# Performance work log

Hardware: AMD Instinct MI355X
Metric: run time of the kernel (lower is better)

Reference implementation:

```python
import jax, jax.numpy as jnp
import numpy as np

N_NODES = 100000
EPS = 1e-12  # F.normalize eps


def mean_aggregate(x, src, dst):
    # gather source features along edges, segment-mean into destinations
    msg = x[src]                                              # [E, D]
    summed = jax.ops.segment_sum(msg, dst, num_segments=N_NODES)  # [N, D]
    cnt = jax.ops.segment_sum(jnp.ones_like(dst, dtype=x.dtype), dst,
                              num_segments=N_NODES)           # [N]
    return summed / jnp.maximum(cnt, 1.0)[:, None]


def sage_conv(x, src, dst, W_l, b_l, W_r, normalize):
    agg = mean_aggregate(x, src, dst)
    out = agg @ W_l.T + b_l + x @ W_r.T  # lin_l(mean neigh) + lin_r(root)
    if normalize:
        norm = jnp.sqrt(jnp.sum(out * out, axis=-1, keepdims=True))
        out = out / jnp.maximum(norm, EPS)
    return out


def setup_inputs() -> dict:
    key = jax.random.key(0)
    ks = jax.random.split(key, 8)
    H, O = 128, 128
    s = 1.0 / np.sqrt(H)
    x = jax.random.normal(ks[0], (N_NODES, H), dtype=jnp.float32)
    edge_index = jax.random.randint(ks[1], (2, 1600000), 0, N_NODES, dtype=jnp.int64)
    return {
        "x": x,
        "edge_index": edge_index,
        "W1l": jax.random.uniform(ks[2], (H, H), jnp.float32, -s, s),
        "b1": jax.random.uniform(ks[3], (H,), jnp.float32, -s, s),
        "W1r": jax.random.uniform(ks[4], (H, H), jnp.float32, -s, s),
        "W2l": jax.random.uniform(ks[5], (O, H), jnp.float32, -s, s),
        "b2": jax.random.uniform(ks[6], (O,), jnp.float32, -s, s),
        "W2r": jax.random.uniform(ks[7], (O, H), jnp.float32, -s, s),
    }


def reference(x, edge_index, W1l, b1, W1r, W2l, b2, W2r):
    src, dst = edge_index[0], edge_index[1]
    h = sage_conv(x, src, dst, W1l, b1, W1r, normalize=True)
    h = jax.nn.relu(h)
    out = sage_conv(h, src, dst, W2l, b2, W2r, normalize=False)
    return out
```

## Files before the change

kernel.cpp:

```cpp
#include <hip/hip_runtime.h>
#include <hip/hip_bf16.h>
#include <hip/hip_fp16.h>

#define N_NODES 100000
#define DFEAT 128
#define SLAB 4096
#define BSHIFT 9
#define NBUCK 196

#define WS_CNT      0
#define WS_W16      100000
#define WS_BCNT     180000
#define WS_BBASE    180200
#define WS_BCUR     180400
#define WS_OFFS     200000
#define WS_ESRC     300608
#define WS_AGGH     1900608
#define WS_CASTH    8300608

typedef _Float16 half8 __attribute__((ext_vector_type(8)));
typedef _Float16 half2v __attribute__((ext_vector_type(2)));
typedef float floatx4 __attribute__((ext_vector_type(4)));

__global__ __launch_bounds__(256) void prep_kernel(const float* __restrict__ x,
                                                   __half* __restrict__ xh, int total4,
                                                   const int* __restrict__ dst,
                                                   int* __restrict__ bcnt,
                                                   const float* __restrict__ W1l,
                                                   const float* __restrict__ W1r,
                                                   const float* __restrict__ W2l,
                                                   const float* __restrict__ W2r,
                                                   __half* __restrict__ w16,
                                                   int E, int bpart, int castblocks) {
    __shared__ int lh[NBUCK];
    int b = blockIdx.x;
    if (b < castblocks) {
        int i = b * 256 + threadIdx.x;
        if (i < total4) {
            float4 v = ((const float4*)x)[i];
            __half2 h01 = __floats2half2_rn(v.x, v.y);
            __half2 h23 = __floats2half2_rn(v.z, v.w);
            uint2 o;
            o.x = *(unsigned int*)&h01;
            o.y = *(unsigned int*)&h23;
            ((uint2*)xh)[i] = o;
        }
        return;
    }
    if (b < castblocks + 64) {
        int i = (b - castblocks) * 256 + threadIdx.x;
        int m = i >> 12;
        int off = i & 4095;
        const float* Wp = (m == 0) ? W1l : (m == 1) ? W1r : (m == 2) ? W2l : W2r;
        float4 v = ((const float4*)Wp)[off];
        __half2 h01 = __floats2half2_rn(v.x, v.y);
        __half2 h23 = __floats2half2_rn(v.z, v.w);
        uint2 o;
        o.x = *(unsigned int*)&h01;
        o.y = *(unsigned int*)&h23;
        ((uint2*)w16)[i] = o;
        return;
    }
    int bb = b - castblocks - 64;
    for (int i = threadIdx.x; i < NBUCK; i += 256) lh[i] = 0;
    __syncthreads();
    int s0 = bb * SLAB, s1 = min(E, s0 + SLAB);
    for (int i = s0 + threadIdx.x; i < s1; i += 256)
        atomicAdd(&lh[dst[i] >> BSHIFT], 1);
    __syncthreads();
    for (int i = threadIdx.x; i < NBUCK; i += 256)
        if (lh[i] > 0) atomicAdd(&bcnt[i], lh[i]);
}

__global__ void bscan_kernel(const int* __restrict__ bcnt, int* __restrict__ bbase,
                             int* __restrict__ bcur, int E) {
    __shared__ int s[256];
    int t = threadIdx.x;
    int v = (t < NBUCK) ? bcnt[t] : 0;
    s[t] = v;
    __syncthreads();
    for (int d = 1; d < 256; d <<= 1) {
        int u = (t >= d) ? s[t - d] : 0;
        __syncthreads();
        s[t] += u;
        __syncthreads();
    }
    if (t < NBUCK) {
        int excl = s[t] - v;
        bbase[t] = excl;
        bcur[t] = excl;
    }
    if (t == 0) bbase[NBUCK] = E;
}

__global__ __launch_bounds__(256) void phase2_kernel(const int* __restrict__ src,
                                                     const int* __restrict__ dst,
                                                     int* __restrict__ bcur,
                                                     int2* __restrict__ pairs,
                                                     int E) {
    __shared__ int lbase[NBUCK];
    __shared__ int lcur[NBUCK];
    __shared__ int lgb[NBUCK];
    __shared__ int sc[256];
    __shared__ int2 lp[SLAB];
    int b = blockIdx.x;
    int t = threadIdx.x;
    for (int i = t; i < NBUCK; i += 256) lbase[i] = 0;
    __syncthreads();
    int s0 = b * SLAB, s1 = min(E, s0 + SLAB);
    for (int i = s0 + t; i < s1; i += 256)
        atomicAdd(&lbase[dst[i] >> BSHIFT], 1);
    __syncthreads();
    int v = (t < NBUCK) ? lbase[t] : 0;
    sc[t] = v;
    __syncthreads();
    for (int d = 1; d < 256; d <<= 1) {
        int u = (t >= d) ? sc[t - d] : 0;
        __syncthreads();
        sc[t] += u;
        __syncthreads();
    }
    if (t < NBUCK) {
        int excl = sc[t] - v;
        lbase[t] = excl;
        lcur[t] = excl;
        lgb[t] = (v > 0) ? atomicAdd(&bcur[t], v) : 0;
    }
    __syncthreads();
    for (int i = s0 + t; i < s1; i += 256) {
        int d = dst[i];
        int s = src[i];
        int bk = d >> BSHIFT;
        int pos = atomicAdd(&lcur[bk], 1);
        lp[pos] = make_int2(s, d);
    }
    __syncthreads();
    int m = s1 - s0;
    for (int i = t; i < m; i += 256) {
        int2 p = lp[i];
        int bk = p.y >> BSHIFT;
        pairs[lgb[bk] + (i - lbase[bk])] = p;
    }
}

__global__ __launch_bounds__(512) void phase3_kernel(const int2* __restrict__ pairs,
                                                     const int* __restrict__ bbase,
                                                     int* __restrict__ cnt,
                                                     int* __restrict__ offs,
                                                     int* __restrict__ esrc,
                                                     int n) {
    __shared__ int lcnt[512];
    __shared__ int sc[512];
    __shared__ int lexcl[512];
    int g = blockIdx.x;
    int node0 = g << BSHIFT;
    int t = threadIdx.x;
    lcnt[t] = 0;
    __syncthreads();
    int S = bbase[g];
    int Eg = bbase[g + 1];
    for (int i = S + t; i < Eg; i += 512)
        atomicAdd(&lcnt[pairs[i].y - node0], 1);
    __syncthreads();
    int v = lcnt[t];
    sc[t] = v;
    __syncthreads();
    for (int d = 1; d < 512; d <<= 1) {
        int u = (t >= d) ? sc[t - d] : 0;
        __syncthreads();
        sc[t] += u;
        __syncthreads();
    }
    int excl = sc[t] - v;
    lexcl[t] = excl;
    int nd = node0 + t;
    if (nd < n) {
        cnt[nd] = v;
        offs[nd] = S + excl;
    }
    __syncthreads();
    for (int i = S + t; i < Eg; i += 512) {
        int2 p = pairs[i];
        int pos = atomicAdd(&lexcl[p.y - node0], 1);
        esrc[S + pos] = p.x;
    }
}

#define ACC(c, r)                        \
    s[c][0] += *(half2v*)&(r).x;         \
    s[c][1] += *(half2v*)&(r).y;         \
    s[c][2] += *(half2v*)&(r).z;         \
    s[c][3] += *(half2v*)&(r).w;

__global__ void aggregate_kernel(const __half* __restrict__ feat, const int* __restrict__ esrc,
                                 const int* __restrict__ offs, const int* __restrict__ cnt,
                                 __half* __restrict__ agg, int n) {
    int wid = (blockIdx.x * blockDim.x + threadIdx.x) >> 6;
    int lane = threadIdx.x & 63;
    int grp = lane >> 4;
    int l15 = lane & 15;
    int node = wid * 4 + grp;
    if (node >= n) return;
    int beg = offs[node];
    int deg = cnt[node];
    const _Float16* fbase = (const _Float16*)feat + l15 * 8;
    const int* ep = esrc + beg;

    half2v s[4][4];
#pragma unroll
    for (int c = 0; c < 4; c++)
#pragma unroll
        for (int k = 0; k < 4; k++) s[c][k] = (half2v)(_Float16)0;

    int j = 0;
    for (; j + 8 <= deg; j += 8) {
        int i0 = ep[j + 0], i1 = ep[j + 1], i2 = ep[j + 2], i3 = ep[j + 3];
        int i4 = ep[j + 4], i5 = ep[j + 5], i6 = ep[j + 6], i7 = ep[j + 7];
        uint4 r0 = *(const uint4*)(fbase + (size_t)i0 * DFEAT);
        uint4 r1 = *(const uint4*)(fbase + (size_t)i1 * DFEAT);
        uint4 r2 = *(const uint4*)(fbase + (size_t)i2 * DFEAT);
        uint4 r3 = *(const uint4*)(fbase + (size_t)i3 * DFEAT);
        uint4 r4 = *(const uint4*)(fbase + (size_t)i4 * DFEAT);
        uint4 r5 = *(const uint4*)(fbase + (size_t)i5 * DFEAT);
        uint4 r6 = *(const uint4*)(fbase + (size_t)i6 * DFEAT);
        uint4 r7 = *(const uint4*)(fbase + (size_t)i7 * DFEAT);
        ACC(0, r0) ACC(1, r1) ACC(2, r2) ACC(3, r3)
        ACC(0, r4) ACC(1, r5) ACC(2, r6) ACC(3, r7)
    }
    for (; j + 4 <= deg; j += 4) {
        int i0 = ep[j + 0], i1 = ep[j + 1], i2 = ep[j + 2], i3 = ep[j + 3];
        uint4 r0 = *(const uint4*)(fbase + (size_t)i0 * DFEAT);
        uint4 r1 = *(const uint4*)(fbase + (size_t)i1 * DFEAT);
        uint4 r2 = *(const uint4*)(fbase + (size_t)i2 * DFEAT);
        uint4 r3 = *(const uint4*)(fbase + (size_t)i3 * DFEAT);
        ACC(0, r0) ACC(1, r1) ACC(2, r2) ACC(3, r3)
    }
    if (j < deg) {
        int rem = deg - j;
        int i0 = ep[j];
        int i1 = ep[j + (rem > 1 ? 1 : 0)];
        int i2 = ep[j + (rem > 2 ? 2 : 0)];
        uint4 r0 = *(const uint4*)(fbase + (size_t)i0 * DFEAT);
        uint4 r1 = *(const uint4*)(fbase + (size_t)i1 * DFEAT);
        uint4 r2 = *(const uint4*)(fbase + (size_t)i2 * DFEAT);
        if (rem < 2) { r1.x = 0u; r1.y = 0u; r1.z = 0u; r1.w = 0u; }
        if (rem < 3) { r2.x = 0u; r2.y = 0u; r2.z = 0u; r2.w = 0u; }
        ACC(0, r0) ACC(1, r1) ACC(2, r2)
    }

    float scale = 1.0f / fmaxf((float)deg, 1.0f);
    float a[8];
#pragma unroll
    for (int k = 0; k < 4; k++) {
        a[2 * k]     = ((float)s[0][k].x + (float)s[1][k].x) + ((float)s[2][k].x + (float)s[3][k].x);
        a[2 * k + 1] = ((float)s[0][k].y + (float)s[1][k].y) + ((float)s[2][k].y + (float)s[3][k].y);
    }
    __half2 h0 = __floats2half2_rn(a[0] * scale, a[1] * scale);
    __half2 h1 = __floats2half2_rn(a[2] * scale, a[3] * scale);
    __half2 h2 = __floats2half2_rn(a[4] * scale, a[5] * scale);
    __half2 h3 = __floats2half2_rn(a[6] * scale, a[7] * scale);
    uint4 o;
    o.x = *(unsigned int*)&h0;
    o.y = *(unsigned int*)&h1;
    o.z = *(unsigned int*)&h2;
    o.w = *(unsigned int*)&h3;
    *(uint4*)(agg + (size_t)node * DFEAT + l15 * 8) = o;
}

template <bool NORM_RELU>
__global__ __launch_bounds__(256) void gemm64_kernel(
    const __half* __restrict__ A1_, const __half* __restrict__ A2_,
    const __half* __restrict__ Wl16, const __half* __restrict__ Wr16,
    const float* __restrict__ bias, float* __restrict__ out32,
    __half* __restrict__ out16, int n) {
    __shared__ __align__(16) _Float16 lw[128 * 136];

    const _Float16* A1 = (const _Float16*)A1_;
    const _Float16* A2 = (const _Float16*)A2_;
    const _Float16* wl = (const _Float16*)Wl16;
    const _Float16* wr = (const _Float16*)Wr16;

    const int lane = threadIdx.x & 63;
    const int w = threadIdx.x >> 6;
    const int quad = lane >> 4;
    const int l15 = lane & 15;
    const int i0 = blockIdx.x * 64 + w * 16;
    int r = i0 + l15;
    if (r >= n) r = n - 1;
    const int kq = quad * 8;

    half8 bf[4];
#pragma unroll
    for (int k = 0; k < 4; k++)
        bf[k] = *(const half8*)(A1 + (size_t)r * DFEAT + k * 32 + kq);

    {
        int t = threadIdx.x;
        int row = t >> 1;
        int cb = (t & 1) * 64;
        const uint4* sp = (const uint4*)(wl + row * DFEAT + cb);
        uint4* dp = (uint4*)&lw[row * 136 + cb];
#pragma unroll
        for (int q = 0; q < 8; q++) dp[q] = sp[q];
    }
    __syncthreads();

    floatx4 acc[8];
#pragma unroll
    for (int ft = 0; ft < 8; ft++) acc[ft] = (floatx4){0.f, 0.f, 0.f, 0.f};

#pragma unroll
    for (int kci = 0; kci < 4; kci++) {
#pragma unroll
        for (int ft = 0; ft < 8; ft++) {
            half8 a = *(const half8*)&lw[(ft * 16 + l15) * 136 + kci * 32 + kq];
            acc[ft] = __builtin_amdgcn_mfma_f32_16x16x32_f16(a, bf[kci], acc[ft], 0, 0, 0);
        }
    }

    half8 xf[4];
#pragma unroll
    for (int k = 0; k < 4; k++)
        xf[k] = *(const half8*)(A2 + (size_t)r * DFEAT + k * 32 + kq);

    __syncthreads();
    {
        int t = threadIdx.x;
        int row = t >> 1;
        int cb = (t & 1) * 64;
        const uint4* sp = (const uint4*)(wr + row * DFEAT + cb);
        uint4* dp = (uint4*)&lw[row * 136 + cb];
#pragma unroll
        for (int q = 0; q < 8; q++) dp[q] = sp[q];
    }
    __syncthreads();

#pragma unroll
    for (int kci = 0; kci < 4; kci++) {
#pragma unroll
        for (int ft = 0; ft < 8; ft++) {
            half8 a = *(const half8*)&lw[(ft * 16 + l15) * 136 + kci * 32 + kq];
            acc[ft] = __builtin_amdgcn_mfma_f32_16x16x32_f16(a, xf[kci], acc[ft], 0, 0, 0);
        }
    }

    int node = i0 + l15;
    float v[8][4];
#pragma unroll
    for (int ft = 0; ft < 8; ft++) {
        const float4 bq = *(const float4*)(bias + ft * 16 + quad * 4);
        v[ft][0] = acc[ft][0] + bq.x;
        v[ft][1] = acc[ft][1] + bq.y;
        v[ft][2] = acc[ft][2] + bq.z;
        v[ft][3] = acc[ft][3] + bq.w;
    }
    if (NORM_RELU) {
        float ss = 0.f;
#pragma unroll
        for (int ft = 0; ft < 8; ft++)
#pragma unroll
            for (int q = 0; q < 4; q++) ss = fmaf(v[ft][q], v[ft][q], ss);
        ss += __shfl_xor(ss, 16);
        ss += __shfl_xor(ss, 32);
        float inv = 1.0f / fmaxf(sqrtf(ss), 1e-12f);
#pragma unroll
        for (int ft = 0; ft < 8; ft++)
#pragma unroll
            for (int q = 0; q < 4; q++) v[ft][q] = fmaxf(v[ft][q] * inv, 0.0f);
    }
    if (node < n) {
        if (NORM_RELU) {
            __half* op = (__half*)out16 + (size_t)node * DFEAT + quad * 4;
#pragma unroll
            for (int ft = 0; ft < 8; ft++) {
                __half2 h01 = __floats2half2_rn(v[ft][0], v[ft][1]);
                __half2 h23 = __floats2half2_rn(v[ft][2], v[ft][3]);
                uint2 o;
                o.x = *(unsigned int*)&h01;
                o.y = *(unsigned int*)&h23;
                *(uint2*)(op + ft * 16) = o;
            }
        } else {
            float* op = out32 + (size_t)node * DFEAT + quad * 4;
#pragma unroll
            for (int ft = 0; ft < 8; ft++)
                *(float4*)(op + ft * 16) = make_float4(v[ft][0], v[ft][1], v[ft][2], v[ft][3]);
        }
    }
}

extern "C" void kernel_launch(void* const* d_in, const int* in_sizes, int n_in,
                              void* d_out, int out_size, void* d_ws, size_t ws_size,
                              hipStream_t stream) {
    const float* x = (const float*)d_in[0];
    const int* edge_index = (const int*)d_in[1];
    const float* W1l = (const float*)d_in[2];
    const float* b1 = (const float*)d_in[3];
    const float* W1r = (const float*)d_in[4];
    const float* W2l = (const float*)d_in[5];
    const float* b2 = (const float*)d_in[6];
    const float* W2r = (const float*)d_in[7];
    float* out = (float*)d_out;

    const int E = in_sizes[1] / 2;
    const int n = in_sizes[0] / DFEAT;

    int* ws = (int*)d_ws;
    int* cnt = ws + WS_CNT;
    __half* w16 = (__half*)(ws + WS_W16);
    int* bcnt = ws + WS_BCNT;
    int* bbase = ws + WS_BBASE;
    int* bcur = ws + WS_BCUR;
    int* offs = ws + WS_OFFS;
    int* esrc = ws + WS_ESRC;
    int2* pairs = (int2*)(ws + WS_AGGH);
    __half* aggh = (__half*)(ws + WS_AGGH);
    __half* casth = (__half*)(ws + WS_CASTH);

    const int* src = edge_index;
    const int* dst = edge_index + E;

    const int bpart = (E + SLAB - 1) / SLAB;
    const int total4 = n * DFEAT / 4;
    const int castblocks = (total4 + 255) / 256;

    __half* w1l16 = w16;
    __half* w1r16 = w16 + 16384;
    __half* w2l16 = w16 + 32768;
    __half* w2r16 = w16 + 49152;

    hipMemsetAsync(bcnt, 0, NBUCK * sizeof(int), stream);

    prep_kernel<<<castblocks + 64 + bpart, 256, 0, stream>>>(
        x, casth, total4, dst, bcnt, W1l, W1r, W2l, W2r, w16, E, bpart, castblocks);
    bscan_kernel<<<1, 256, 0, stream>>>(bcnt, bbase, bcur, E);
    phase2_kernel<<<bpart, 256, 0, stream>>>(src, dst, bcur, pairs, E);
    phase3_kernel<<<NBUCK, 512, 0, stream>>>(pairs, bbase, cnt, offs, esrc, n);

    const int nwaves = (n + 3) / 4;
    const int aggb = (nwaves * 64 + 255) / 256;
    const int gemmb = (n + 63) / 64;

    aggregate_kernel<<<aggb, 256, 0, stream>>>(casth, esrc, offs, cnt, aggh, n);
    gemm64_kernel<true><<<gemmb, 256, 0, stream>>>(aggh, casth, w1l16, w1r16, b1,
                                                   nullptr, aggh, n);

    aggregate_kernel<<<aggb, 256, 0, stream>>>(aggh, esrc, offs, cnt, casth, n);
    gemm64_kernel<false><<<gemmb, 256, 0, stream>>>(casth, aggh, w2l16, w2r16, b2,
                                                    out, nullptr, n);
}
```

Measured before the change: 341.1 us.

## Pack bucketed edge pairs into 32-bit words and split prep kernel

Intermediate bucketed edge pairs are packed into a single int (local dst offset in the high bits, src in the low 17 bits) instead of int2, which halves the pair traffic written by phase2 and read twice by phase3. The combined prep kernel is split into separate cast-x (grid-stride), cast-weights and histogram kernels, and the block sizes of the histogram, phase2 and phase3 kernels are raised. The packing relies on node ids fitting in 17 bits and on 512-node buckets. The split also adds two extra kernel launches.

```diff
diff --git a/kernel.cpp b/kernel.cpp
--- a/kernel.cpp
+++ b/kernel.cpp
@@ -22,54 +22,49 @@
 typedef _Float16 half2v __attribute__((ext_vector_type(2)));
 typedef float floatx4 __attribute__((ext_vector_type(4)));
 
-__global__ __launch_bounds__(256) void prep_kernel(const float* __restrict__ x,
-                                                   __half* __restrict__ xh, int total4,
-                                                   const int* __restrict__ dst,
-                                                   int* __restrict__ bcnt,
-                                                   const float* __restrict__ W1l,
-                                                   const float* __restrict__ W1r,
-                                                   const float* __restrict__ W2l,
-                                                   const float* __restrict__ W2r,
-                                                   __half* __restrict__ w16,
-                                                   int E, int bpart, int castblocks) {
-    __shared__ int lh[NBUCK];
-    int b = blockIdx.x;
-    if (b < castblocks) {
-        int i = b * 256 + threadIdx.x;
-        if (i < total4) {
-            float4 v = ((const float4*)x)[i];
-            __half2 h01 = __floats2half2_rn(v.x, v.y);
-            __half2 h23 = __floats2half2_rn(v.z, v.w);
-            uint2 o;
-            o.x = *(unsigned int*)&h01;
-            o.y = *(unsigned int*)&h23;
-            ((uint2*)xh)[i] = o;
-        }
-        return;
-    }
-    if (b < castblocks + 64) {
-        int i = (b - castblocks) * 256 + threadIdx.x;
-        int m = i >> 12;
-        int off = i & 4095;
-        const float* Wp = (m == 0) ? W1l : (m == 1) ? W1r : (m == 2) ? W2l : W2r;
-        float4 v = ((const float4*)Wp)[off];
+__global__ __launch_bounds__(256) void cast_x_kernel(const float* __restrict__ x,
+                                                     __half* __restrict__ xh, int total4) {
+    int stride = gridDim.x * 256;
+    for (int i = blockIdx.x * 256 + threadIdx.x; i < total4; i += stride) {
+        float4 v = ((const float4*)x)[i];
         __half2 h01 = __floats2half2_rn(v.x, v.y);
         __half2 h23 = __floats2half2_rn(v.z, v.w);
         uint2 o;
         o.x = *(unsigned int*)&h01;
         o.y = *(unsigned int*)&h23;
-        ((uint2*)w16)[i] = o;
-        return;
-    }
-    int bb = b - castblocks - 64;
-    for (int i = threadIdx.x; i < NBUCK; i += 256) lh[i] = 0;
-    __syncthreads();
-    int s0 = bb * SLAB, s1 = min(E, s0 + SLAB);
-    for (int i = s0 + threadIdx.x; i < s1; i += 256)
+        ((uint2*)xh)[i] = o;
+    }
+}
+
+__global__ __launch_bounds__(256) void cast_w_kernel(const float* __restrict__ W1l,
+                                                     const float* __restrict__ W1r,
+                                                     const float* __restrict__ W2l,
+                                                     const float* __restrict__ W2r,
+                                                     __half* __restrict__ w16) {
+    int i = blockIdx.x * 256 + threadIdx.x;
+    int m = i >> 12;
+    int off = i & 4095;
+    const float* Wp = (m == 0) ? W1l : (m == 1) ? W1r : (m == 2) ? W2l : W2r;
+    float4 v = ((const float4*)Wp)[off];
+    __half2 h01 = __floats2half2_rn(v.x, v.y);
+    __half2 h23 = __floats2half2_rn(v.z, v.w);
+    uint2 o;
+    o.x = *(unsigned int*)&h01;
+    o.y = *(unsigned int*)&h23;
+    ((uint2*)w16)[i] = o;
+}
+
+__global__ __launch_bounds__(1024) void hist_kernel(const int* __restrict__ dst,
+                                                    int* __restrict__ bcnt, int E) {
+    __shared__ int lh[NBUCK];
+    int t = threadIdx.x;
+    if (t < NBUCK) lh[t] = 0;
+    __syncthreads();
+    int s0 = blockIdx.x * SLAB, s1 = min(E, s0 + SLAB);
+    for (int i = s0 + t; i < s1; i += 1024)
         atomicAdd(&lh[dst[i] >> BSHIFT], 1);
     __syncthreads();
-    for (int i = threadIdx.x; i < NBUCK; i += 256)
-        if (lh[i] > 0) atomicAdd(&bcnt[i], lh[i]);
+    if (t < NBUCK && lh[t] > 0) atomicAdd(&bcnt[t], lh[t]);
 }
 
 __global__ void bscan_kernel(const int* __restrict__ bcnt, int* __restrict__ bbase,
@@ -93,10 +88,10 @@
     if (t == 0) bbase[NBUCK] = E;
 }
 
-__global__ __launch_bounds__(256) void phase2_kernel(const int* __restrict__ src,
+__global__ __launch_bounds__(512) void phase2_kernel(const int* __restrict__ src,
                                                      const int* __restrict__ dst,
                                                      int* __restrict__ bcur,
-                                                     int2* __restrict__ pairs,
+                                                     int* __restrict__ pairs,
                                                      int E) {
     __shared__ int lbase[NBUCK];
     __shared__ int lcur[NBUCK];
@@ -105,19 +100,19 @@
     __shared__ int2 lp[SLAB];
     int b = blockIdx.x;
     int t = threadIdx.x;
-    for (int i = t; i < NBUCK; i += 256) lbase[i] = 0;
+    if (t < NBUCK) lbase[t] = 0;
     __syncthreads();
     int s0 = b * SLAB, s1 = min(E, s0 + SLAB);
-    for (int i = s0 + t; i < s1; i += 256)
+    for (int i = s0 + t; i < s1; i += 512)
         atomicAdd(&lbase[dst[i] >> BSHIFT], 1);
     __syncthreads();
     int v = (t < NBUCK) ? lbase[t] : 0;
-    sc[t] = v;
+    if (t < 256) sc[t] = v;
     __syncthreads();
     for (int d = 1; d < 256; d <<= 1) {
-        int u = (t >= d) ? sc[t - d] : 0;
-        __syncthreads();
-        sc[t] += u;
+        int u = (t >= d && t < 256) ? sc[t - d] : 0;
+        __syncthreads();
+        if (t < 256) sc[t] += u;
         __syncthreads();
     }
     if (t < NBUCK) {
@@ -127,7 +122,7 @@
         lgb[t] = (v > 0) ? atomicAdd(&bcur[t], v) : 0;
     }
     __syncthreads();
-    for (int i = s0 + t; i < s1; i += 256) {
+    for (int i = s0 + t; i < s1; i += 512) {
         int d = dst[i];
         int s = src[i];
         int bk = d >> BSHIFT;
@@ -136,53 +131,55 @@
     }
     __syncthreads();
     int m = s1 - s0;
-    for (int i = t; i < m; i += 256) {
+    for (int i = t; i < m; i += 512) {
         int2 p = lp[i];
         int bk = p.y >> BSHIFT;
-        pairs[lgb[bk] + (i - lbase[bk])] = p;
-    }
-}
-
-__global__ __launch_bounds__(512) void phase3_kernel(const int2* __restrict__ pairs,
-                                                     const int* __restrict__ bbase,
-                                                     int* __restrict__ cnt,
-                                                     int* __restrict__ offs,
-                                                     int* __restrict__ esrc,
-                                                     int n) {
+        pairs[lgb[bk] + (i - lbase[bk])] = ((p.y & 511) << 17) | p.x;
+    }
+}
+
+__global__ __launch_bounds__(1024) void phase3_kernel(const int* __restrict__ pairs,
+                                                      const int* __restrict__ bbase,
+                                                      int* __restrict__ cnt,
+                                                      int* __restrict__ offs,
+                                                      int* __restrict__ esrc,
+                                                      int n) {
     __shared__ int lcnt[512];
     __shared__ int sc[512];
     __shared__ int lexcl[512];
     int g = blockIdx.x;
     int node0 = g << BSHIFT;
     int t = threadIdx.x;
-    lcnt[t] = 0;
+    if (t < 512) lcnt[t] = 0;
     __syncthreads();
     int S = bbase[g];
     int Eg = bbase[g + 1];
-    for (int i = S + t; i < Eg; i += 512)
-        atomicAdd(&lcnt[pairs[i].y - node0], 1);
-    __syncthreads();
-    int v = lcnt[t];
-    sc[t] = v;
+    for (int i = S + t; i < Eg; i += 1024)
+        atomicAdd(&lcnt[pairs[i] >> 17], 1);
+    __syncthreads();
+    int v = (t < 512) ? lcnt[t] : 0;
+    if (t < 512) sc[t] = v;
     __syncthreads();
     for (int d = 1; d < 512; d <<= 1) {
-        int u = (t >= d) ? sc[t - d] : 0;
-        __syncthreads();
-        sc[t] += u;
-        __syncthreads();
-    }
-    int excl = sc[t] - v;
-    lexcl[t] = excl;
-    int nd = node0 + t;
-    if (nd < n) {
-        cnt[nd] = v;
-        offs[nd] = S + excl;
-    }
-    __syncthreads();
-    for (int i = S + t; i < Eg; i += 512) {
-        int2 p = pairs[i];
-        int pos = atomicAdd(&lexcl[p.y - node0], 1);
-        esrc[S + pos] = p.x;
+        int u = (t >= d && t < 512) ? sc[t - d] : 0;
+        __syncthreads();
+        if (t < 512) sc[t] += u;
+        __syncthreads();
+    }
+    if (t < 512) {
+        int excl = sc[t] - v;
+        lexcl[t] = excl;
+        int nd = node0 + t;
+        if (nd < n) {
+            cnt[nd] = v;
+            offs[nd] = S + excl;
+        }
+    }
+    __syncthreads();
+    for (int i = S + t; i < Eg; i += 1024) {
+        int p = pairs[i];
+        int pos = atomicAdd(&lexcl[p >> 17], 1);
+        esrc[S + pos] = p & 0x1FFFF;
     }
 }
 
@@ -413,7 +410,7 @@
     int* bcur = ws + WS_BCUR;
     int* offs = ws + WS_OFFS;
     int* esrc = ws + WS_ESRC;
-    int2* pairs = (int2*)(ws + WS_AGGH);
+    int* pairs = ws + WS_AGGH;
     __half* aggh = (__half*)(ws + WS_AGGH);
     __half* casth = (__half*)(ws + WS_CASTH);
 
@@ -422,7 +419,6 @@
 
     const int bpart = (E + SLAB - 1) / SLAB;
     const int total4 = n * DFEAT / 4;
-    const int castblocks = (total4 + 255) / 256;
 
     __half* w1l16 = w16;
     __half* w1r16 = w16 + 16384;
@@ -431,11 +427,12 @@
 
     hipMemsetAsync(bcnt, 0, NBUCK * sizeof(int), stream);
 
-    prep_kernel<<<castblocks + 64 + bpart, 256, 0, stream>>>(
-        x, casth, total4, dst, bcnt, W1l, W1r, W2l, W2r, w16, E, bpart, castblocks);
+    cast_x_kernel<<<2048, 256, 0, stream>>>(x, casth, total4);
+    cast_w_kernel<<<64, 256, 0, stream>>>(W1l, W1r, W2l, W2r, w16);
+    hist_kernel<<<bpart, 1024, 0, stream>>>(dst, bcnt, E);
     bscan_kernel<<<1, 256, 0, stream>>>(bcnt, bbase, bcur, E);
-    phase2_kernel<<<bpart, 256, 0, stream>>>(src, dst, bcur, pairs, E);
-    phase3_kernel<<<NBUCK, 512, 0, stream>>>(pairs, bbase, cnt, offs, esrc, n);
+    phase2_kernel<<<bpart, 512, 0, stream>>>(src, dst, bcur, pairs, E);
+    phase3_kernel<<<NBUCK, 1024, 0, stream>>>(pairs, bbase, cnt, offs, esrc, n);
 
     const int nwaves = (n + 3) / 4;
     const int aggb = (nwaves * 64 + 255) / 256;
```

Result: faster. 329.7 us (-3.3%).
